# Performance work log

Measured on AMD Instinct MI355X. Metric: run time of the kernel, lower is better.

The kernel has to match this reference:

```python
import jax, jax.numpy as jnp
import numpy as np

N_NODES = 100000
N_EDGES = 1000000
D_IN = 64
D_OUT = 64


def setup_inputs() -> dict:
    key = jax.random.key(0)
    k_x, k_e, k_wl, k_bl, k_wr = jax.random.split(key, 5)
    x = jax.random.normal(k_x, (N_NODES, D_IN), dtype=jnp.float32)
    edge_index = jax.random.randint(k_e, (2, N_EDGES), 0, N_NODES, dtype=jnp.int64)
    scale = 1.0 / np.sqrt(D_IN)
    # SAGEConv params: lin_l (neighbor path, with bias), lin_r (root/self path, no bias)
    W_l = jax.random.uniform(k_wl, (D_OUT, D_IN), dtype=jnp.float32, minval=-scale, maxval=scale)
    b_l = jax.random.uniform(k_bl, (D_OUT,), dtype=jnp.float32, minval=-scale, maxval=scale)
    W_r = jax.random.uniform(k_wr, (D_OUT, D_IN), dtype=jnp.float32, minval=-scale, maxval=scale)
    return {"x": x, "edge_index": edge_index, "W_l": W_l, "b_l": b_l, "W_r": W_r}


def reference(x, edge_index, W_l, b_l, W_r):
    # PyG SAGEConv with mean aggregation:
    #   out = lin_l(mean_{j in N(i)} x_j) + lin_r(x_i);  then ReLU (from GCN.forward)
    src = edge_index[0]  # message sources
    dst = edge_index[1]  # aggregation targets
    n = x.shape[0]
    msg = x[src]  # [E, D_IN] gather
    agg = jax.ops.segment_sum(msg, dst, num_segments=n)  # [N, D_IN]
    deg = jax.ops.segment_sum(jnp.ones((src.shape[0],), x.dtype), dst, num_segments=n)
    mean = agg / jnp.maximum(deg, 1.0)[:, None]  # isolated nodes -> 0
    out = mean @ W_l.T + b_l + x @ W_r.T
    return jax.nn.relu(out)
```

## Files before the change

### kernel.cpp

```cpp
#include <hip/hip_runtime.h>

#define N_NODES 100000
#define N_EDGES 1000000
#define D 64

#define NFINE 782
#define CAP2 1536
#define CHUNK 8192
#define EDGE_BLOCKS 123
#define CONV_BLOCKS 6250
#define CONS_BLOCKS 3125
#define STR 132

typedef unsigned short u16;
typedef unsigned int u32;
using bf16x8 = __attribute__((ext_vector_type(8))) short;
using f32x4  = __attribute__((ext_vector_type(4))) float;

__device__ __forceinline__ u16 f2bf(float f) {
    u32 u = __float_as_uint(f);
    return (u16)((u + 0x7FFF + ((u >> 16) & 1)) >> 16);
}
__device__ __forceinline__ float bf2f(u16 v) {
    return __uint_as_float(((u32)v) << 16);
}

__global__ __launch_bounds__(256) void conv_zero_kernel(
    const float* __restrict__ x, u16* __restrict__ xb,
    int* __restrict__ cur2) {
    if (blockIdx.x == CONV_BLOCKS) {
        for (int j = threadIdx.x; j < NFINE; j += 256) cur2[j] = 0;
        return;
    }
    int i = blockIdx.x * 256 + threadIdx.x;
    float4 v = ((const float4*)x)[i];
    ((ushort4*)xb)[i] = make_ushort4(f2bf(v.x), f2bf(v.y), f2bf(v.z), f2bf(v.w));
}

__global__ __launch_bounds__(1024) void build3_kernel(
    const int* __restrict__ ei, int* __restrict__ cur2,
    u32* __restrict__ pairs2) {
    __shared__ u32 sorted[CHUNK];
    __shared__ u16 binof[CHUNK];
    __shared__ int hist[NFINE];
    __shared__ int off_l[NFINE];
    __shared__ int cur_l[NFINE];
    __shared__ int base_g[NFINE];

    int b = blockIdx.x;
    int t = threadIdx.x;

    const u32* uu = (const u32*)ei;
    int f = 1;
    #pragma unroll
    for (int i = 1; i < 16; i += 2)
        if (uu[i] != 0u) f = 0;

    if (t < NFINE) hist[t] = 0;
    __syncthreads();

    int e0 = b * CHUNK;
    int e1 = min(e0 + CHUNK, N_EDGES);
    int ne = e1 - e0;

    for (int e = e0 + t; e < e1; e += 1024) {
        int dst = f ? ei[2 * (N_EDGES + e)] : ei[N_EDGES + e];
        atomicAdd(&hist[dst >> 7], 1);
    }
    __syncthreads();

    if (t < NFINE) off_l[t] = hist[t];
    __syncthreads();
    #pragma unroll
    for (int off = 1; off < 1024; off <<= 1) {
        int v = 0;
        if (t < NFINE && t >= off) v = off_l[t - off];
        __syncthreads();
        if (t < NFINE) off_l[t] += v;
        __syncthreads();
        if (off >= NFINE) break;
    }
    if (t < NFINE) {
        int h = hist[t];
        int ex = off_l[t] - h;
        off_l[t] = ex;
        cur_l[t] = ex;
        base_g[t] = h ? atomicAdd(&cur2[t], h) : 0;
    }
    __syncthreads();

    for (int e = e0 + t; e < e1; e += 1024) {
        int src = f ? ei[2 * e] : ei[e];
        int dst = f ? ei[2 * (N_EDGES + e)] : ei[N_EDGES + e];
        int fine = dst >> 7;
        int slot = atomicAdd(&cur_l[fine], 1);
        sorted[slot] = (u32)src | ((u32)(dst & 127) << 17);
        binof[slot] = (u16)fine;
    }
    __syncthreads();

    for (int i = t; i < ne; i += 1024) {
        int fine = binof[i];
        int pos = base_g[fine] + (i - off_l[fine]);
        if (pos < CAP2)
            pairs2[(size_t)fine * CAP2 + pos] = sorted[i];
    }
}

__global__ __launch_bounds__(256) void cons2_kernel(
    const u16* __restrict__ xb, const float* __restrict__ Wl,
    const float* __restrict__ bl, const float* __restrict__ Wr,
    const int* __restrict__ cur2, const u32* __restrict__ pairs2,
    float* __restrict__ out) {
    __shared__ u16 Bs[64 * STR];
    __shared__ u16 As[32 * STR];
    __shared__ int sorted_s[512];
    __shared__ int deg_l[32];
    __shared__ int off_l[32];
    __shared__ int cur_l[32];
    __shared__ int scan_s[32];

    int tid = threadIdx.x;
    int bin = blockIdx.x >> 2;
    int sub = blockIdx.x & 3;
    int nbase = bin * 128 + sub * 32;
    if (nbase >= N_NODES) return;

    int lane = tid & 63;
    int wv = tid >> 6;

    if (tid < 32) { deg_l[tid] = 0; cur_l[tid] = 0; }

    {
        int row = tid >> 2;
        int seg = tid & 3;
        const float4* wlf = (const float4*)Wl;
        const float4* wrf = (const float4*)Wr;
        #pragma unroll
        for (int j = 0; j < 4; j++) {
            float4 a = wlf[row * 16 + seg * 4 + j];
            float4 bq = wrf[row * 16 + seg * 4 + j];
            *(ushort4*)&Bs[row * STR + seg * 16 + j * 4] =
                make_ushort4(f2bf(a.x), f2bf(a.y), f2bf(a.z), f2bf(a.w));
            *(ushort4*)&Bs[row * STR + 64 + seg * 16 + j * 4] =
                make_ushort4(f2bf(bq.x), f2bf(bq.y), f2bf(bq.z), f2bf(bq.w));
        }
    }
    __syncthreads();

    int cnt = min(cur2[bin], CAP2);
    const u32* pb = &pairs2[(size_t)bin * CAP2];
    u32 ve[6];
    int nev = 0;
    for (int e = tid; e < cnt; e += 256) ve[nev++] = pb[e];

    for (int i = 0; i < nev; i++) {
        u32 dl = ve[i] >> 17;
        if ((int)(dl >> 5) == sub) atomicAdd(&deg_l[dl & 31], 1);
    }
    __syncthreads();
    if (tid < 32) scan_s[tid] = deg_l[tid];
    __syncthreads();
    #pragma unroll
    for (int off = 1; off < 32; off <<= 1) {
        int v = 0;
        if (tid < 32 && tid >= off) v = scan_s[tid - off];
        __syncthreads();
        if (tid < 32) scan_s[tid] += v;
        __syncthreads();
    }
    if (tid < 32) off_l[tid] = scan_s[tid] - deg_l[tid];
    __syncthreads();
    for (int i = 0; i < nev; i++) {
        u32 v = ve[i];
        u32 dl = v >> 17;
        if ((int)(dl >> 5) == sub) {
            int ln = dl & 31;
            int p = off_l[ln] + atomicAdd(&cur_l[ln], 1);
            if (p < 512) sorted_s[p] = (int)(v & 0x1FFFFu);
        }
    }
    __syncthreads();

    int nl8 = lane >> 3;
    int c = lane & 7;
    int nl = wv * 8 + nl8;
    int n = nbase + nl;
    int d = deg_l[nl];
    int st = off_l[nl];

    int maxd = d;
    maxd = max(maxd, __shfl_xor(maxd, 8));
    maxd = max(maxd, __shfl_xor(maxd, 16));
    maxd = max(maxd, __shfl_xor(maxd, 32));

    float acc[8];
    #pragma unroll
    for (int j = 0; j < 8; j++) acc[j] = 0.0f;

    for (int k = 0; k < maxd; k++) {
        int idx = (st + min(k, d - 1)) & 511;
        int s = sorted_s[idx];
        float m = (k < d) ? 1.0f : 0.0f;
        bf16x8 r = *(const bf16x8*)&xb[(size_t)s * D + c * 8];
        #pragma unroll
        for (int j = 0; j < 8; j++)
            acc[j] = fmaf(m, bf2f((u16)r[j]), acc[j]);
    }

    float inv = (d > 0) ? (1.0f / (float)d) : 0.0f;
    bf16x8 p;
    #pragma unroll
    for (int j = 0; j < 8; j++) p[j] = (short)f2bf(acc[j] * inv);
    *(bf16x8*)&As[nl * STR + c * 8] = p;
    bf16x8 xr = *(const bf16x8*)&xb[(size_t)n * D + c * 8];
    *(bf16x8*)&As[nl * STR + 64 + c * 8] = xr;
    __syncthreads();

    int mtile = wv >> 1;
    int nt0 = (wv & 1) * 2;
    int lrow = lane & 15;
    int quad = lane >> 4;

    const u16* Ab  = &As[(mtile * 16 + lrow) * STR + quad * 8];
    const u16* Bb0 = &Bs[((nt0 + 0) * 16 + lrow) * STR + quad * 8];
    const u16* Bb1 = &Bs[((nt0 + 1) * 16 + lrow) * STR + quad * 8];

    float bias0 = bl[(nt0 + 0) * 16 + lrow];
    float bias1 = bl[(nt0 + 1) * 16 + lrow];
    f32x4 acc0 = {bias0, bias0, bias0, bias0};
    f32x4 acc1 = {bias1, bias1, bias1, bias1};

    #pragma unroll
    for (int kk = 0; kk < 4; kk++) {
        bf16x8 af = *(const bf16x8*)&Ab[kk * 32];
        bf16x8 b0 = *(const bf16x8*)&Bb0[kk * 32];
        bf16x8 b1 = *(const bf16x8*)&Bb1[kk * 32];
        acc0 = __builtin_amdgcn_mfma_f32_16x16x32_bf16(af, b0, acc0, 0, 0, 0);
        acc1 = __builtin_amdgcn_mfma_f32_16x16x32_bf16(af, b1, acc1, 0, 0, 0);
    }

    int node = nbase + mtile * 16 + quad * 4;
    #pragma unroll
    for (int r = 0; r < 4; r++) {
        out[(size_t)(node + r) * D + (nt0 + 0) * 16 + lrow] = fmaxf(acc0[r], 0.0f);
        out[(size_t)(node + r) * D + (nt0 + 1) * 16 + lrow] = fmaxf(acc1[r], 0.0f);
    }
}

extern "C" void kernel_launch(void* const* d_in, const int* in_sizes, int n_in,
                              void* d_out, int out_size, void* d_ws, size_t ws_size,
                              hipStream_t stream) {
    const float* x  = (const float*)d_in[0];
    const int*   ei = (const int*)d_in[1];
    const float* Wl = (const float*)d_in[2];
    const float* bl = (const float*)d_in[3];
    const float* Wr = (const float*)d_in[4];
    float* out = (float*)d_out;

    char* p = (char*)d_ws;
    int* cur2   = (int*)p;                        p += 1024 * sizeof(int);
    u32* pairs2 = (u32*)p;                        p += (size_t)NFINE * CAP2 * sizeof(u32);
    u16* xb     = (u16*)p;

    conv_zero_kernel<<<CONV_BLOCKS + 1, 256, 0, stream>>>(x, xb, cur2);
    build3_kernel<<<EDGE_BLOCKS, 1024, 0, stream>>>(ei, cur2, pairs2);
    cons2_kernel<<<CONS_BLOCKS, 256, 0, stream>>>(xb, Wl, bl, Wr, cur2, pairs2, out);
}
```

Before: 146.2 us.

## Process full bins per 1024-thread block and use wave-shuffle scans in build

The consumer kernel now handles a whole 128-node bin in one 1024-thread block, so each bin's edge list is read and sorted once instead of four times. The build kernel halves its chunk size to launch twice as many blocks, keeps edges in registers between the histogram and scatter passes, and replaces the barrier-heavy shared-memory scan with wave shuffle scans. The gather loop is unrolled by two to put more loads in flight. The cost is fewer and larger consumer blocks with more shared memory, which can hurt occupancy and tail balance, and the previous 512-entry sort cap is removed.

```diff
diff --git a/kernel.cpp b/kernel.cpp
--- a/kernel.cpp
+++ b/kernel.cpp
@@ -6,10 +6,10 @@
 
 #define NFINE 782
 #define CAP2 1536
-#define CHUNK 8192
-#define EDGE_BLOCKS 123
+#define CHUNK 4096
+#define EDGE_BLOCKS 245
 #define CONV_BLOCKS 6250
-#define CONS_BLOCKS 3125
+#define CONS_BLOCKS 782
 #define STR 132
 
 typedef unsigned short u16;
@@ -46,9 +46,12 @@
     __shared__ int off_l[NFINE];
     __shared__ int cur_l[NFINE];
     __shared__ int base_g[NFINE];
+    __shared__ int wsum[16];
 
     int b = blockIdx.x;
     int t = threadIdx.x;
+    int ln = t & 63;
+    int wv = t >> 6;
 
     const u32* uu = (const u32*)ei;
     int f = 1;
@@ -63,39 +66,55 @@
     int e1 = min(e0 + CHUNK, N_EDGES);
     int ne = e1 - e0;
 
-    for (int e = e0 + t; e < e1; e += 1024) {
-        int dst = f ? ei[2 * (N_EDGES + e)] : ei[N_EDGES + e];
-        atomicAdd(&hist[dst >> 7], 1);
-    }
-    __syncthreads();
-
-    if (t < NFINE) off_l[t] = hist[t];
-    __syncthreads();
-    #pragma unroll
-    for (int off = 1; off < 1024; off <<= 1) {
-        int v = 0;
-        if (t < NFINE && t >= off) v = off_l[t - off];
-        __syncthreads();
-        if (t < NFINE) off_l[t] += v;
-        __syncthreads();
-        if (off >= NFINE) break;
-    }
+    int srcv[4], dstv[4];
+    #pragma unroll
+    for (int i = 0; i < 4; i++) {
+        int ee = e0 + t + i * 1024;
+        bool ok = ee < e1;
+        srcv[i] = ok ? (f ? ei[2 * ee] : ei[ee]) : 0;
+        dstv[i] = ok ? (f ? ei[2 * (N_EDGES + ee)] : ei[N_EDGES + ee]) : -1;
+    }
+    #pragma unroll
+    for (int i = 0; i < 4; i++)
+        if (dstv[i] >= 0) atomicAdd(&hist[dstv[i] >> 7], 1);
+    __syncthreads();
+
+    int h = (t < NFINE) ? hist[t] : 0;
+    int inc = h;
+    #pragma unroll
+    for (int o = 1; o < 64; o <<= 1) {
+        int v = __shfl_up(inc, o);
+        if (ln >= o) inc += v;
+    }
+    if (ln == 63) wsum[wv] = inc;
+    __syncthreads();
+    if (t < 16) {
+        int w = wsum[t];
+        int winc = w;
+        #pragma unroll
+        for (int o = 1; o < 16; o <<= 1) {
+            int v = __shfl_up(winc, o);
+            if (t >= o) winc += v;
+        }
+        wsum[t] = winc - w;
+    }
+    __syncthreads();
     if (t < NFINE) {
-        int h = hist[t];
-        int ex = off_l[t] - h;
+        int ex = inc - h + wsum[wv];
         off_l[t] = ex;
         cur_l[t] = ex;
         base_g[t] = h ? atomicAdd(&cur2[t], h) : 0;
     }
     __syncthreads();
 
-    for (int e = e0 + t; e < e1; e += 1024) {
-        int src = f ? ei[2 * e] : ei[e];
-        int dst = f ? ei[2 * (N_EDGES + e)] : ei[N_EDGES + e];
-        int fine = dst >> 7;
-        int slot = atomicAdd(&cur_l[fine], 1);
-        sorted[slot] = (u32)src | ((u32)(dst & 127) << 17);
-        binof[slot] = (u16)fine;
+    #pragma unroll
+    for (int i = 0; i < 4; i++) {
+        if (dstv[i] >= 0) {
+            int fine = dstv[i] >> 7;
+            int slot = atomicAdd(&cur_l[fine], 1);
+            sorted[slot] = (u32)srcv[i] | ((u32)(dstv[i] & 127) << 17);
+            binof[slot] = (u16)fine;
+        }
     }
     __syncthreads();
 
@@ -107,31 +126,28 @@
     }
 }
 
-__global__ __launch_bounds__(256) void cons2_kernel(
+__global__ __launch_bounds__(1024, 8) void cons3_kernel(
     const u16* __restrict__ xb, const float* __restrict__ Wl,
     const float* __restrict__ bl, const float* __restrict__ Wr,
     const int* __restrict__ cur2, const u32* __restrict__ pairs2,
     float* __restrict__ out) {
     __shared__ u16 Bs[64 * STR];
-    __shared__ u16 As[32 * STR];
-    __shared__ int sorted_s[512];
-    __shared__ int deg_l[32];
-    __shared__ int off_l[32];
-    __shared__ int cur_l[32];
-    __shared__ int scan_s[32];
+    __shared__ u16 As[128 * STR];
+    __shared__ int sorted_s[CAP2];
+    __shared__ int deg_l[128];
+    __shared__ int off_l[128];
+    __shared__ int cur_l[128];
 
     int tid = threadIdx.x;
-    int bin = blockIdx.x >> 2;
-    int sub = blockIdx.x & 3;
-    int nbase = bin * 128 + sub * 32;
-    if (nbase >= N_NODES) return;
-
+    int bin = blockIdx.x;
+    int nbase = bin * 128;
     int lane = tid & 63;
     int wv = tid >> 6;
 
-    if (tid < 32) { deg_l[tid] = 0; cur_l[tid] = 0; }
-
-    {
+    if (tid < 128) { deg_l[tid] = 0; cur_l[tid] = 0; }
+    for (int i = tid; i < CAP2; i += 1024) sorted_s[i] = 0;
+
+    if (tid < 256) {
         int row = tid >> 2;
         int seg = tid & 3;
         const float4* wlf = (const float4*)Wl;
@@ -146,38 +162,44 @@
                 make_ushort4(f2bf(bq.x), f2bf(bq.y), f2bf(bq.z), f2bf(bq.w));
         }
     }
-    __syncthreads();
 
     int cnt = min(cur2[bin], CAP2);
     const u32* pb = &pairs2[(size_t)bin * CAP2];
-    u32 ve[6];
-    int nev = 0;
-    for (int e = tid; e < cnt; e += 256) ve[nev++] = pb[e];
-
-    for (int i = 0; i < nev; i++) {
-        u32 dl = ve[i] >> 17;
-        if ((int)(dl >> 5) == sub) atomicAdd(&deg_l[dl & 31], 1);
-    }
-    __syncthreads();
-    if (tid < 32) scan_s[tid] = deg_l[tid];
-    __syncthreads();
-    #pragma unroll
-    for (int off = 1; off < 32; off <<= 1) {
-        int v = 0;
-        if (tid < 32 && tid >= off) v = scan_s[tid - off];
-        __syncthreads();
-        if (tid < 32) scan_s[tid] += v;
-        __syncthreads();
-    }
-    if (tid < 32) off_l[tid] = scan_s[tid] - deg_l[tid];
-    __syncthreads();
-    for (int i = 0; i < nev; i++) {
+    u32 ve[2];
+    #pragma unroll
+    for (int i = 0; i < 2; i++) {
+        int e = tid + i * 1024;
+        ve[i] = (e < cnt) ? pb[e] : 0xFFFFFFFFu;
+    }
+    __syncthreads();
+
+    #pragma unroll
+    for (int i = 0; i < 2; i++)
+        if (ve[i] != 0xFFFFFFFFu) atomicAdd(&deg_l[ve[i] >> 17], 1);
+    __syncthreads();
+
+    if (tid < 64) {
+        int d0 = deg_l[2 * tid], d1 = deg_l[2 * tid + 1];
+        int s = d0 + d1;
+        int inc = s;
+        #pragma unroll
+        for (int o = 1; o < 64; o <<= 1) {
+            int v = __shfl_up(inc, o);
+            if (tid >= o) inc += v;
+        }
+        int ex = inc - s;
+        off_l[2 * tid] = ex;
+        off_l[2 * tid + 1] = ex + d0;
+    }
+    __syncthreads();
+
+    #pragma unroll
+    for (int i = 0; i < 2; i++) {
         u32 v = ve[i];
-        u32 dl = v >> 17;
-        if ((int)(dl >> 5) == sub) {
-            int ln = dl & 31;
-            int p = off_l[ln] + atomicAdd(&cur_l[ln], 1);
-            if (p < 512) sorted_s[p] = (int)(v & 0x1FFFFu);
+        if (v != 0xFFFFFFFFu) {
+            int dl = (int)(v >> 17);
+            int p = off_l[dl] + atomicAdd(&cur_l[dl], 1);
+            sorted_s[p] = (int)(v & 0x1FFFFu);
         }
     }
     __syncthreads();
@@ -198,14 +220,21 @@
     #pragma unroll
     for (int j = 0; j < 8; j++) acc[j] = 0.0f;
 
-    for (int k = 0; k < maxd; k++) {
-        int idx = (st + min(k, d - 1)) & 511;
-        int s = sorted_s[idx];
-        float m = (k < d) ? 1.0f : 0.0f;
-        bf16x8 r = *(const bf16x8*)&xb[(size_t)s * D + c * 8];
+    for (int k = 0; k < maxd; k += 2) {
+        int i0 = max(st + min(k, d - 1), 0);
+        int i1 = max(st + min(k + 1, d - 1), 0);
+        int s0 = sorted_s[i0];
+        int s1 = sorted_s[i1];
+        float m0 = (k < d) ? 1.0f : 0.0f;
+        float m1 = (k + 1 < d) ? 1.0f : 0.0f;
+        bf16x8 r0 = *(const bf16x8*)&xb[(size_t)s0 * D + c * 8];
+        bf16x8 r1 = *(const bf16x8*)&xb[(size_t)s1 * D + c * 8];
         #pragma unroll
         for (int j = 0; j < 8; j++)
-            acc[j] = fmaf(m, bf2f((u16)r[j]), acc[j]);
+            acc[j] = fmaf(m0, bf2f((u16)r0[j]), acc[j]);
+        #pragma unroll
+        for (int j = 0; j < 8; j++)
+            acc[j] = fmaf(m1, bf2f((u16)r1[j]), acc[j]);
     }
 
     float inv = (d > 0) ? (1.0f / (float)d) : 0.0f;
@@ -213,7 +242,8 @@
     #pragma unroll
     for (int j = 0; j < 8; j++) p[j] = (short)f2bf(acc[j] * inv);
     *(bf16x8*)&As[nl * STR + c * 8] = p;
-    bf16x8 xr = *(const bf16x8*)&xb[(size_t)n * D + c * 8];
+    bf16x8 xr = {0, 0, 0, 0, 0, 0, 0, 0};
+    if (n < N_NODES) xr = *(const bf16x8*)&xb[(size_t)n * D + c * 8];
     *(bf16x8*)&As[nl * STR + 64 + c * 8] = xr;
     __syncthreads();
 
@@ -243,8 +273,10 @@
     int node = nbase + mtile * 16 + quad * 4;
     #pragma unroll
     for (int r = 0; r < 4; r++) {
-        out[(size_t)(node + r) * D + (nt0 + 0) * 16 + lrow] = fmaxf(acc0[r], 0.0f);
-        out[(size_t)(node + r) * D + (nt0 + 1) * 16 + lrow] = fmaxf(acc1[r], 0.0f);
+        if (node + r < N_NODES) {
+            out[(size_t)(node + r) * D + (nt0 + 0) * 16 + lrow] = fmaxf(acc0[r], 0.0f);
+            out[(size_t)(node + r) * D + (nt0 + 1) * 16 + lrow] = fmaxf(acc1[r], 0.0f);
+        }
     }
 }
 
@@ -265,5 +297,5 @@
 
     conv_zero_kernel<<<CONV_BLOCKS + 1, 256, 0, stream>>>(x, xb, cur2);
     build3_kernel<<<EDGE_BLOCKS, 1024, 0, stream>>>(ei, cur2, pairs2);
-    cons2_kernel<<<CONS_BLOCKS, 256, 0, stream>>>(xb, Wl, bl, Wr, cur2, pairs2, out);
-}
+    cons3_kernel<<<CONS_BLOCKS, 1024, 0, stream>>>(xb, Wl, bl, Wr, cur2, pairs2, out);
+}
```

Result: faster. 143.0 us (-2.2%).
